# Optimization experiments

Measured on AMD Instinct MI355X. Metric: run time of the kernel, lower is better.

## Reference

```python
import jax, jax.numpy as jnp
import numpy as np
jax.config.update("jax_enable_x64", True)

PAD_ID = -1
NUM_DISCRETE = 128  # args.n_discrete_size

def _lexsort3(v):
    # torch code: stable argsort by x, then y, then z -> final key order z (primary), y, x.
    # numpy/jax lexsort: last key is primary, and it is stable.
    idx = jnp.lexsort((v[:, 0], v[:, 1], v[:, 2]))
    return v[idx], idx

def setup_inputs() -> dict:
    key = jax.random.key(0)
    k1, k2 = jax.random.split(key)
    B, NV, NF = 32, 32768, 65536
    vertices = jax.random.normal(k1, (B, NV, 3), dtype=jnp.float32)
    faces = jax.random.randint(k2, (B, NF, 3), 0, NV, dtype=jnp.int64)
    n_pad = NF // 10
    faces = faces.at[:, NF - n_pad:, :].set(PAD_ID)
    return {"vertices": vertices, "faces": faces}

def reference(vertices, faces):
    B, NV, _ = vertices.shape
    # normalize_vertices reduces over dim 0 (which is the BATCH dim here) - faithful to source
    mn = vertices.min(axis=0)
    mx = vertices.max(axis=0)
    center = (mn + mx) * 0.5
    longest = (mx - mn).max()
    v = (vertices - center) / longest
    # batched lexicographic sort of vertices
    sorted_v, sort_idx = jax.vmap(_lexsort3)(v)
    # inverse permutation (inv[sort_idx] = arange  <=>  argsort of a permutation)
    inv = jnp.argsort(sort_idx, axis=1)  # (B, NV)
    # torch indexes inverse_mapping[faces] with pad -1 wrapping to NV-1
    wrapped = jnp.mod(faces, NV)
    reindexed = jax.vmap(lambda m, f: m[f])(inv, wrapped)  # (B, NF, 3)
    sorted_faces, _ = jax.vmap(_lexsort3)(reindexed)
    # face mask: all three vertex ids != pad
    face_mask = jnp.all(faces != PAD_ID, axis=-1)  # (B, NF)
    face_np = jnp.where(face_mask[..., None], faces, 0)
    # gather vertex coords per face: (B, NF, 3verts, 3coords). The torch code
    # materializes a (b,nf,nv,3) repeat then gathers; we gather directly.
    face_coords = jax.vmap(lambda vv, ff: vv[ff])(sorted_v, face_np)
    # discretize into [-1, 1] -> [0, 127]
    t = (face_coords + 1.0) * 0.5 * NUM_DISCRETE - 0.5
    dq = jnp.clip(jnp.round(t).astype(jnp.int64), 0, NUM_DISCRETE - 1)
    codes = jnp.where(face_mask[..., None, None], dq, PAD_ID)
    input_ids = codes.reshape(B, -1)
    attention_mask = (input_ids != PAD_ID).astype(jnp.float32)
    ph = jnp.full((B, 1), PAD_ID, dtype=input_ids.dtype)
    input_ids = jnp.concatenate([ph, input_ids, ph], axis=1)
    attention_mask = jnp.concatenate([ph.astype(jnp.float32), attention_mask, ph.astype(jnp.float32)], axis=1)
    return input_ids, attention_mask, codes, dq, sorted_faces
```

## Files before the change

### kernel.cpp

```cpp
#include <hip/hip_runtime.h>
#include <stdint.h>

#define BATCH 32
#define NV 32768
#define NF 65536
#define PCOUNT (NV*3)


__device__ __forceinline__ unsigned fenc(float f){
  unsigned u = __float_as_uint(f);
  return (u & 0x80000000u) ? ~u : (u | 0x80000000u);
}
__device__ __forceinline__ float fdec(unsigned e){
  unsigned u = (e & 0x80000000u) ? (e & 0x7FFFFFFFu) : ~e;
  return __uint_as_float(u);
}

__global__ void kminmax(const float* __restrict__ vert, float* __restrict__ center,
                        unsigned* __restrict__ longestBits){
  int p = blockIdx.x*256 + threadIdx.x;
  float mn = 3.4e38f, mx = -3.4e38f;
  #pragma unroll
  for (int b = 0; b < BATCH; ++b) {
    float v = vert[(size_t)b*PCOUNT + p];
    mn = fminf(mn, v); mx = fmaxf(mx, v);
  }
  center[p] = __fadd_rn(mn, mx) * 0.5f;
  float r = __fsub_rn(mx, mn);
  for (int off = 32; off > 0; off >>= 1) r = fmaxf(r, __shfl_down(r, off, 64));
  if ((threadIdx.x & 63) == 0) atomicMax(longestBits, __float_as_uint(r));
}

__device__ __forceinline__ bool less4(uint4 a, uint4 b){
  if (a.x != b.x) return a.x < b.x;
  if (a.y != b.y) return a.y < b.y;
  if (a.z != b.z) return a.z < b.z;
  return a.w < b.w;
}
__device__ __forceinline__ bool less2(uint2 a, uint2 b){
  if (a.y != b.y) return a.y < b.y;
  return a.x < b.x;
}

#define VT 2048
#define FT 4096
#define SWV(i) ((i) ^ (((i) >> 3) & 7))
#define SWF(i) ((i) ^ (((i) >> 4) & 15))

__global__ __launch_bounds__(256) void klocalv(const float* __restrict__ vert,
                                               const float* __restrict__ center,
                                               const unsigned* __restrict__ longestBits,
                                               uint4* __restrict__ S){
  __shared__ uint4 sh[VT];
  int blockBase = blockIdx.x * VT;
  float L = __uint_as_float(*longestBits);
  float rl = __fdiv_rn(1.0f, L);
  for (int i = threadIdx.x; i < VT; i += 256){
    int id = blockBase + i;
    int vi = id & (NV-1);
    size_t vb = (size_t)(id >> 15)*PCOUNT + (size_t)vi*3;
    float nx = __fsub_rn(vert[vb+0], center[vi*3+0]);
    float ny = __fsub_rn(vert[vb+1], center[vi*3+1]);
    float nz = __fsub_rn(vert[vb+2], center[vi*3+2]);
    float x = __fmul_rn(nx, rl);
    float y = __fmul_rn(ny, rl);
    float z = __fmul_rn(nz, rl);
    uint4 s; s.x = fenc(z); s.y = fenc(y); s.z = fenc(x); s.w = (unsigned)vi;
    sh[SWV(i)] = s;
  }
  __syncthreads();
  int t = threadIdx.x;
  int k0 = t * 8;
  uint4 v[8];
  #pragma unroll
  for (int e = 0; e < 8; ++e) v[e] = sh[SWV(k0 + e)];
  #pragma unroll
  for (int k = 2; k <= 8; k <<= 1){
    #pragma unroll
    for (int j = k >> 1; j > 0; j >>= 1){
      #pragma unroll
      for (int i = 0; i < 8; ++i){
        int l = i ^ j;
        if (l > i){
          bool up = ((i & k) == 0);
          bool sw = up ? less4(v[l], v[i]) : less4(v[i], v[l]);
          if (sw){ uint4 tmp = v[i]; v[i] = v[l]; v[l] = tmp; }
        }
      }
    }
  }
  #pragma unroll
  for (int e = 0; e < 8; ++e) sh[SWV(k0 + e)] = v[e];
  __syncthreads();
  for (int w = 8; w < VT; w <<= 1){
    int base = k0 & ~(2*w - 1);
    int ko = k0 - base;
    int lo = ko - w; if (lo < 0) lo = 0;
    int hi = ko < w ? ko : w;
    while (lo < hi){
      int mid = (lo + hi) >> 1;
      if (less4(sh[SWV(base + mid)], sh[SWV(base + w + ko-1-mid)])) lo = mid + 1; else hi = mid;
    }
    int i = lo, j = ko - lo;
    uint4 m[8];
    #pragma unroll
    for (int e = 0; e < 8; ++e){
      bool takeA = (j >= w) || (i < w && less4(sh[SWV(base + i)], sh[SWV(base + w + j)]));
      m[e] = takeA ? sh[SWV(base + i)] : sh[SWV(base + w + j)];
      if (takeA) ++i; else ++j;
    }
    __syncthreads();
    #pragma unroll
    for (int e = 0; e < 8; ++e) sh[SWV(k0 + e)] = m[e];
    __syncthreads();
  }
  uint4* basep = S + (size_t)blockBase;
  for (int i = threadIdx.x; i < VT; i += 256) basep[i] = sh[SWV(i)];
}

__global__ __launch_bounds__(256) void klocalf(const int* __restrict__ faces,
                                               const int* __restrict__ inv,
                                               uint2* __restrict__ F){
  __shared__ uint2 sh[FT];
  int blockBase = blockIdx.x * FT;
  int b = blockBase >> 16;
  const int* invb = inv + (b << 15);
  for (int i = threadIdx.x; i < FT; i += 256){
    int id = blockBase + i;
    int f = id & (NF-1);
    size_t fb = (size_t)id*3;
    int f0 = faces[fb+0], f1 = faces[fb+1], f2 = faces[fb+2];
    unsigned r0 = (unsigned)invb[f0 & (NV-1)];
    unsigned r1 = (unsigned)invb[f1 & (NV-1)];
    unsigned r2 = (unsigned)invb[f2 & (NV-1)];
    uint2 r; r.x = (r0 << 15) | (unsigned)f; r.y = (r2 << 15) | r1;
    sh[SWF(i)] = r;
  }
  __syncthreads();
  int t = threadIdx.x;
  int k0 = t * 16;
  uint2 v[16];
  #pragma unroll
  for (int e = 0; e < 16; ++e) v[e] = sh[SWF(k0 + e)];
  #pragma unroll
  for (int k = 2; k <= 16; k <<= 1){
    #pragma unroll
    for (int j = k >> 1; j > 0; j >>= 1){
      #pragma unroll
      for (int i = 0; i < 16; ++i){
        int l = i ^ j;
        if (l > i){
          bool up = ((i & k) == 0);
          bool sw = up ? less2(v[l], v[i]) : less2(v[i], v[l]);
          if (sw){ uint2 tmp = v[i]; v[i] = v[l]; v[l] = tmp; }
        }
      }
    }
  }
  #pragma unroll
  for (int e = 0; e < 16; ++e) sh[SWF(k0 + e)] = v[e];
  __syncthreads();
  for (int w = 16; w < FT; w <<= 1){
    int base = k0 & ~(2*w - 1);
    int ko = k0 - base;
    int lo = ko - w; if (lo < 0) lo = 0;
    int hi = ko < w ? ko : w;
    while (lo < hi){
      int mid = (lo + hi) >> 1;
      if (less2(sh[SWF(base + mid)], sh[SWF(base + w + ko-1-mid)])) lo = mid + 1; else hi = mid;
    }
    int i = lo, j = ko - lo;
    uint2 m[16];
    #pragma unroll
    for (int e = 0; e < 16; ++e){
      bool takeA = (j >= w) || (i < w && less2(sh[SWF(base + i)], sh[SWF(base + w + j)]));
      m[e] = takeA ? sh[SWF(base + i)] : sh[SWF(base + w + j)];
      if (takeA) ++i; else ++j;
    }
    __syncthreads();
    #pragma unroll
    for (int e = 0; e < 16; ++e) sh[SWF(k0 + e)] = m[e];
    __syncthreads();
  }
  uint2* basep = F + (size_t)blockBase;
  for (int i = threadIdx.x; i < FT; i += 256) basep[i] = sh[SWF(i)];
}

__global__ __launch_bounds__(256) void kmergev(const uint4* __restrict__ src,
                                               uint4* __restrict__ dst, int L){
  __shared__ uint4 sh[2048];
  __shared__ int sAB[2];
  int gid = blockIdx.x;
  int b = gid >> 4, c = gid & 15;
  const uint4* base = src + ((size_t)b << 15);
  uint4* obase = dst + ((size_t)b << 15);
  int co = c * 2048;
  int pair = co / (2*L);
  int ko = co - pair*2*L;
  const uint4* A = base + (size_t)pair*2*L;
  const uint4* B = A + L;
  uint4* O = obase + (size_t)pair*2*L + ko;
  if (threadIdx.x < 2){
    int k = ko + (int)threadIdx.x * 2048;
    int lo = k - L; if (lo < 0) lo = 0;
    int hi = k < L ? k : L;
    while (lo < hi){
      int mid = (lo + hi) >> 1;
      if (less4(A[mid], B[k-1-mid])) lo = mid + 1; else hi = mid;
    }
    sAB[threadIdx.x] = lo;
  }
  __syncthreads();
  int aStart = sAB[0];
  int na = sAB[1] - aStart;
  int nb = 2048 - na;
  int bStart = ko - aStart;
  for (int i = threadIdx.x; i < 2048; i += 256)
    sh[i] = (i < na) ? A[aStart + i] : B[bStart + (i - na)];
  __syncthreads();
  int k0 = threadIdx.x * 8;
  int lo = k0 - nb; if (lo < 0) lo = 0;
  int hi = k0 < na ? k0 : na;
  while (lo < hi){
    int mid = (lo + hi) >> 1;
    if (less4(sh[mid], sh[na + k0-1-mid])) lo = mid + 1; else hi = mid;
  }
  int i = lo, j = k0 - lo;
  #pragma unroll
  for (int e = 0; e < 8; ++e){
    bool takeA = (j >= nb) || (i < na && less4(sh[i], sh[na + j]));
    uint4 v = takeA ? sh[i] : sh[na + j];
    if (takeA) ++i; else ++j;
    O[k0 + e] = v;
  }
}

__global__ __launch_bounds__(256) void kmergef(const uint2* __restrict__ src,
                                               uint2* __restrict__ dst, int L){
  __shared__ uint2 sh[2048];
  __shared__ int sAB[2];
  int gid = blockIdx.x;
  int b = gid >> 5, c = gid & 31;
  const uint2* base = src + ((size_t)b << 16);
  uint2* obase = dst + ((size_t)b << 16);
  int co = c * 2048;
  int pair = co / (2*L);
  int ko = co - pair*2*L;
  const uint2* A = base + (size_t)pair*2*L;
  const uint2* B = A + L;
  uint2* O = obase + (size_t)pair*2*L + ko;
  if (threadIdx.x < 2){
    int k = ko + (int)threadIdx.x * 2048;
    int lo = k - L; if (lo < 0) lo = 0;
    int hi = k < L ? k : L;
    while (lo < hi){
      int mid = (lo + hi) >> 1;
      if (less2(A[mid], B[k-1-mid])) lo = mid + 1; else hi = mid;
    }
    sAB[threadIdx.x] = lo;
  }
  __syncthreads();
  int aStart = sAB[0];
  int na = sAB[1] - aStart;
  int nb = 2048 - na;
  int bStart = ko - aStart;
  for (int i = threadIdx.x; i < 2048; i += 256)
    sh[i] = (i < na) ? A[aStart + i] : B[bStart + (i - na)];
  __syncthreads();
  int k0 = threadIdx.x * 8;
  int lo = k0 - nb; if (lo < 0) lo = 0;
  int hi = k0 < na ? k0 : na;
  while (lo < hi){
    int mid = (lo + hi) >> 1;
    if (less2(sh[mid], sh[na + k0-1-mid])) lo = mid + 1; else hi = mid;
  }
  int i = lo, j = k0 - lo;
  #pragma unroll
  for (int e = 0; e < 8; ++e){
    bool takeA = (j >= nb) || (i < na && less2(sh[i], sh[na + j]));
    uint2 v = takeA ? sh[i] : sh[na + j];
    if (takeA) ++i; else ++j;
    O[k0 + e] = v;
  }
}

__global__ __launch_bounds__(256) void kmergefOut(const uint2* __restrict__ src,
                                                  float* __restrict__ out){
  __shared__ __align__(16) float shf[6144];
  __shared__ int sAB[2];
  uint2* sh = (uint2*)shf;
  const int L = 32768;
  int gid = blockIdx.x;
  int b = gid >> 5, c = gid & 31;
  const uint2* A = src + ((size_t)b << 16);
  const uint2* B = A + L;
  int ko = c * 2048;
  if (threadIdx.x < 2){
    int k = ko + (int)threadIdx.x * 2048;
    int lo = k - L; if (lo < 0) lo = 0;
    int hi = k < L ? k : L;
    while (lo < hi){
      int mid = (lo + hi) >> 1;
      if (less2(A[mid], B[k-1-mid])) lo = mid + 1; else hi = mid;
    }
    sAB[threadIdx.x] = lo;
  }
  __syncthreads();
  int aStart = sAB[0];
  int na = sAB[1] - aStart;
  int nb = 2048 - na;
  int bStart = ko - aStart;
  for (int i = threadIdx.x; i < 2048; i += 256)
    sh[i] = (i < na) ? A[aStart + i] : B[bStart + (i - na)];
  __syncthreads();
  int k0 = threadIdx.x * 8;
  int lo = k0 - nb; if (lo < 0) lo = 0;
  int hi = k0 < na ? k0 : na;
  while (lo < hi){
    int mid = (lo + hi) >> 1;
    if (less2(sh[mid], sh[na + k0-1-mid])) lo = mid + 1; else hi = mid;
  }
  int i = lo, j = k0 - lo;
  uint2 v[8];
  #pragma unroll
  for (int e = 0; e < 8; ++e){
    bool takeA = (j >= nb) || (i < na && less2(sh[i], sh[na + j]));
    v[e] = takeA ? sh[i] : sh[na + j];
    if (takeA) ++i; else ++j;
  }
  __syncthreads();
  #pragma unroll
  for (int e = 0; e < 8; ++e){
    int o = (k0 + e) * 3;
    shf[o+0] = (float)(v[e].x >> 15);
    shf[o+1] = (float)(v[e].y & 0x7FFFu);
    shf[o+2] = (float)(v[e].y >> 15);
  }
  __syncthreads();
  size_t basef = 75497600 + ((size_t)b*65536 + (size_t)ko)*3;
  for (int q = threadIdx.x; q < 6144; q += 256) out[basef + q] = shf[q];
}

__global__ void kinvq(const uint4* __restrict__ S, int* __restrict__ inv,
                      unsigned* __restrict__ Q){
  #pragma clang fp contract(off)
  int id = blockIdx.x*256 + threadIdx.x;
  int b = id >> 15, j = id & (NV-1);
  uint4 s = S[id];
  inv[(b<<15) + (int)s.w] = j;
  float c[3]; c[0] = fdec(s.z); c[1] = fdec(s.y); c[2] = fdec(s.x);
  unsigned qw = 0;
  #pragma unroll
  for (int cc = 0; cc < 3; ++cc){
    float t = ((c[cc] + 1.0f) * 0.5f) * 128.0f - 0.5f;
    float rq = rintf(t);
    int qi = (int)rq;
    qi = qi < 0 ? 0 : (qi > 127 ? 127 : qi);
    qw |= ((unsigned)qi) << (8*cc);
  }
  Q[id] = qw;
}

__global__ __launch_bounds__(256) void kfacesB(const int* __restrict__ faces,
                                               const unsigned* __restrict__ Q,
                                               float* __restrict__ out){
  __shared__ __align__(16) float shq[2304];
  __shared__ float shm[256];
  int p = blockIdx.x;
  int l = ((p & 7) << 10) | (p >> 3);
  int b = l >> 8, c = l & 255;
  int t = threadIdx.x;
  {
    size_t fb = ((size_t)(l*256 + t))*3;
    int f0 = faces[fb+0], f1 = faces[fb+1], f2 = faces[fb+2];
    bool mask = (f0 != -1) & (f1 != -1) & (f2 != -1);
    shm[t] = mask ? 1.0f : 0.0f;
    int fv[3] = {mask ? f0 : 0, mask ? f1 : 0, mask ? f2 : 0};
    #pragma unroll
    for (int k = 0; k < 3; ++k){
      unsigned qw = Q[(b<<15) + fv[k]];
      shq[t*9 + k*3 + 0] = (float)( qw        & 0xFFu);
      shq[t*9 + k*3 + 1] = (float)((qw >> 8 ) & 0xFFu);
      shq[t*9 + k*3 + 2] = (float)((qw >> 16) & 0xFFu);
    }
  }
  __syncthreads();
  float4* cp = (float4*)(out + 37748864 + (size_t)l*2304);
  float4* dp = (float4*)(out + 56623232 + (size_t)l*2304);
  for (int r = t; r < 576; r += 256){
    int e0 = r*4;
    float4 q = *(const float4*)&shq[e0];
    float m0 = shm[(unsigned)(e0  )/9u];
    float m1 = shm[(unsigned)(e0+1)/9u];
    float m2 = shm[(unsigned)(e0+2)/9u];
    float m3 = shm[(unsigned)(e0+3)/9u];
    float4 cv;
    cv.x = m0 != 0.0f ? q.x : -1.0f;
    cv.y = m1 != 0.0f ? q.y : -1.0f;
    cv.z = m2 != 0.0f ? q.z : -1.0f;
    cv.w = m3 != 0.0f ? q.w : -1.0f;
    cp[r] = cv;
    dp[r] = q;
  }
  size_t idsBase  = (size_t)b*589826 + 1 + (size_t)c*2304;
  size_t attnBase = 18874432 + idsBase;
  #pragma unroll
  for (int r = 0; r < 9; ++r){
    int idx = r*256 + t;
    float q = shq[idx];
    float m = shm[(unsigned)idx/9u];
    float cv = m != 0.0f ? q : -1.0f;
    out[idsBase + idx]  = cv;
    out[attnBase + idx] = m;
  }
  if (c == 0 && t == 0){
    out[(size_t)b*589826]                     = -1.0f;
    out[(size_t)b*589826 + 589825]            = -1.0f;
    out[18874432 + (size_t)b*589826]          = -1.0f;
    out[18874432 + (size_t)b*589826 + 589825] = -1.0f;
  }
}

extern "C" void kernel_launch(void* const* d_in, const int* in_sizes, int n_in,
                              void* d_out, int out_size, void* d_ws, size_t ws_size,
                              hipStream_t stream){
  const float* vert  = (const float*)d_in[0];
  const int*   faces = (const int*)d_in[1];
  float* out = (float*)d_out;

  uint4*    S           = (uint4*)d_ws;
  uint4*    S2          = (uint4*)((char*)d_ws + 16777216);
  uint2*    FKa         = (uint2*)((char*)d_ws + 16777216);
  unsigned* Q           = (unsigned*)((char*)d_ws + 16777216);
  uint2*    FKb         = (uint2*)d_ws;
  int*      inv         = (int*)((char*)d_ws + 33554432);
  float*    center      = (float*)((char*)d_ws + 37748736);
  unsigned* longestBits = (unsigned*)((char*)d_ws + 38141952);

  hipMemsetAsync(longestBits, 0, 4, stream);
  kminmax<<<PCOUNT/256, 256, 0, stream>>>(vert, center, longestBits);

  klocalv<<<BATCH*(NV/VT), 256, 0, stream>>>(vert, center, longestBits, S);
  kmergev<<<BATCH*16, 256, 0, stream>>>(S,  S2, 2048);
  kmergev<<<BATCH*16, 256, 0, stream>>>(S2, S,  4096);
  kmergev<<<BATCH*16, 256, 0, stream>>>(S,  S2, 8192);
  kmergev<<<BATCH*16, 256, 0, stream>>>(S2, S,  16384);

  kinvq<<<(BATCH*NV)/256, 256, 0, stream>>>(S, inv, Q);
  kfacesB<<<(BATCH*NF)/256, 256, 0, stream>>>(faces, Q, out);

  klocalf<<<BATCH*(NF/FT), 256, 0, stream>>>(faces, inv, FKa);
  kmergef<<<BATCH*32, 256, 0, stream>>>(FKa, FKb, 4096);
  kmergef<<<BATCH*32, 256, 0, stream>>>(FKb, FKa, 8192);
  kmergef<<<BATCH*32, 256, 0, stream>>>(FKa, FKb, 16384);
  kmergefOut<<<BATCH*32, 256, 0, stream>>>(FKb, out);
}
```

Baseline: 674.8 us.

## Double local sort tile size and fuse final vertex merge with inverse/quantize

Block-local sort tiles double (vertices 4096, faces 8192) with 512 threads per block, so each sort needs one fewer global merge pass. The last vertex merge pass writes the inverse permutation and the quantized coordinates directly, which removes the separate kinvq kernel and a full read of the sorted buffer. The cost is larger shared memory per block (64 KB for vertices), which lowers occupancy for the local sorts. The hidden body of the local sort must also handle the larger tile.

Result: faster. 643.1 us (-4.7%).

```diff
diff --git a/kernel.cpp b/kernel.cpp
--- a/kernel.cpp
+++ b/kernel.cpp
@@ -42,12 +42,12 @@
   return a.x < b.x;
 }
 
-#define VT 2048
-#define FT 4096
+#define VT 4096
+#define FT 8192
 #define SWV(i) ((i) ^ (((i) >> 3) & 7))
 #define SWF(i) ((i) ^ (((i) >> 4) & 15))
 
-__global__ __launch_bounds__(256) void klocalv(const float* __restrict__ vert,
+__global__ __launch_bounds__(512) void klocalv(const float* __restrict__ vert,
                                                const float* __restrict__ center,
                                                const unsigned* __restrict__ longestBits,
                                                uint4* __restrict__ S){
@@ -55,7 +55,7 @@
   int blockBase = blockIdx.x * VT;
   float L = __uint_as_float(*longestBits);
   float rl = __fdiv_rn(1.0f, L);
-  for (int i = threadIdx.x; i < VT; i += 256){
+  for (int i = threadIdx.x; i < VT; i += 512){
     int id = blockBase + i;
     int vi = id & (NV-1);
     size_t vb = (size_t)(id >> 15)*PCOUNT + (size_t)vi*3;
@@ -115,17 +115,17 @@
     __syncthreads();
   }
   uint4* basep = S + (size_t)blockBase;
-  for (int i = threadIdx.x; i < VT; i += 256) basep[i] = sh[SWV(i)];
-}
-
-__global__ __launch_bounds__(256) void klocalf(const int* __restrict__ faces,
+  for (int i = threadIdx.x; i < VT; i += 512) basep[i] = sh[SWV(i)];
+}
+
+__global__ __launch_bounds__(512) void klocalf(const int* __restrict__ faces,
                                                const int* __restrict__ inv,
                                                uint2* __restrict__ F){
   __shared__ uint2 sh[FT];
   int blockBase = blockIdx.x * FT;
   int b = blockBase >> 16;
   const int* invb = inv + (b << 15);
-  for (int i = threadIdx.x; i < FT; i += 256){
+  for (int i = threadIdx.x; i < FT; i += 512){
     int id = blockBase + i;
     int f = id & (NF-1);
     size_t fb = (size_t)id*3;
@@ -183,7 +183,7 @@
     __syncthreads();
   }
   uint2* basep = F + (size_t)blockBase;
-  for (int i = threadIdx.x; i < FT; i += 256) basep[i] = sh[SWF(i)];
+  for (int i = threadIdx.x; i < FT; i += 512) basep[i] = sh[SWF(i)];
 }
 
 __global__ __launch_bounds__(256) void kmergev(const uint4* __restrict__ src,
@@ -235,6 +235,65 @@
   }
 }
 
+__global__ __launch_bounds__(256) void kmergevQ(const uint4* __restrict__ src,
+                                                int* __restrict__ inv,
+                                                unsigned* __restrict__ Q){
+  #pragma clang fp contract(off)
+  __shared__ uint4 sh[2048];
+  __shared__ int sAB[2];
+  const int L = 16384;
+  int gid = blockIdx.x;
+  int b = gid >> 4, c = gid & 15;
+  const uint4* A = src + ((size_t)b << 15);
+  const uint4* B = A + L;
+  int ko = c * 2048;
+  if (threadIdx.x < 2){
+    int k = ko + (int)threadIdx.x * 2048;
+    int lo = k - L; if (lo < 0) lo = 0;
+    int hi = k < L ? k : L;
+    while (lo < hi){
+      int mid = (lo + hi) >> 1;
+      if (less4(A[mid], B[k-1-mid])) lo = mid + 1; else hi = mid;
+    }
+    sAB[threadIdx.x] = lo;
+  }
+  __syncthreads();
+  int aStart = sAB[0];
+  int na = sAB[1] - aStart;
+  int nb = 2048 - na;
+  int bStart = ko - aStart;
+  for (int i = threadIdx.x; i < 2048; i += 256)
+    sh[i] = (i < na) ? A[aStart + i] : B[bStart + (i - na)];
+  __syncthreads();
+  int k0 = threadIdx.x * 8;
+  int lo = k0 - nb; if (lo < 0) lo = 0;
+  int hi = k0 < na ? k0 : na;
+  while (lo < hi){
+    int mid = (lo + hi) >> 1;
+    if (less4(sh[mid], sh[na + k0-1-mid])) lo = mid + 1; else hi = mid;
+  }
+  int i = lo, j = k0 - lo;
+  #pragma unroll
+  for (int e = 0; e < 8; ++e){
+    bool takeA = (j >= nb) || (i < na && less4(sh[i], sh[na + j]));
+    uint4 s = takeA ? sh[i] : sh[na + j];
+    if (takeA) ++i; else ++j;
+    int pos = ko + k0 + e;
+    inv[(b<<15) + (int)s.w] = pos;
+    float cco[3]; cco[0] = fdec(s.z); cco[1] = fdec(s.y); cco[2] = fdec(s.x);
+    unsigned qw = 0;
+    #pragma unroll
+    for (int cc = 0; cc < 3; ++cc){
+      float tt = ((cco[cc] + 1.0f) * 0.5f) * 128.0f - 0.5f;
+      float rq = rintf(tt);
+      int qi = (int)rq;
+      qi = qi < 0 ? 0 : (qi > 127 ? 127 : qi);
+      qw |= ((unsigned)qi) << (8*cc);
+    }
+    Q[(b<<15) + pos] = qw;
+  }
+}
+
 __global__ __launch_bounds__(256) void kmergef(const uint2* __restrict__ src,
                                                uint2* __restrict__ dst, int L){
   __shared__ uint2 sh[2048];
@@ -341,26 +400,6 @@
   for (int q = threadIdx.x; q < 6144; q += 256) out[basef + q] = shf[q];
 }
 
-__global__ void kinvq(const uint4* __restrict__ S, int* __restrict__ inv,
-                      unsigned* __restrict__ Q){
-  #pragma clang fp contract(off)
-  int id = blockIdx.x*256 + threadIdx.x;
-  int b = id >> 15, j = id & (NV-1);
-  uint4 s = S[id];
-  inv[(b<<15) + (int)s.w] = j;
-  float c[3]; c[0] = fdec(s.z); c[1] = fdec(s.y); c[2] = fdec(s.x);
-  unsigned qw = 0;
-  #pragma unroll
-  for (int cc = 0; cc < 3; ++cc){
-    float t = ((c[cc] + 1.0f) * 0.5f) * 128.0f - 0.5f;
-    float rq = rintf(t);
-    int qi = (int)rq;
-    qi = qi < 0 ? 0 : (qi > 127 ? 127 : qi);
-    qw |= ((unsigned)qi) << (8*cc);
-  }
-  Q[id] = qw;
-}
-
 __global__ __launch_bounds__(256) void kfacesB(const int* __restrict__ faces,
                                                const unsigned* __restrict__ Q,
                                                float* __restrict__ out){
@@ -440,18 +479,15 @@
   hipMemsetAsync(longestBits, 0, 4, stream);
   kminmax<<<PCOUNT/256, 256, 0, stream>>>(vert, center, longestBits);
 
-  klocalv<<<BATCH*(NV/VT), 256, 0, stream>>>(vert, center, longestBits, S);
-  kmergev<<<BATCH*16, 256, 0, stream>>>(S,  S2, 2048);
-  kmergev<<<BATCH*16, 256, 0, stream>>>(S2, S,  4096);
-  kmergev<<<BATCH*16, 256, 0, stream>>>(S,  S2, 8192);
-  kmergev<<<BATCH*16, 256, 0, stream>>>(S2, S,  16384);
-
-  kinvq<<<(BATCH*NV)/256, 256, 0, stream>>>(S, inv, Q);
+  klocalv<<<BATCH*(NV/VT), 512, 0, stream>>>(vert, center, longestBits, S);
+  kmergev<<<BATCH*16, 256, 0, stream>>>(S,  S2, 4096);
+  kmergev<<<BATCH*16, 256, 0, stream>>>(S2, S,  8192);
+  kmergevQ<<<BATCH*16, 256, 0, stream>>>(S, inv, Q);
+
   kfacesB<<<(BATCH*NF)/256, 256, 0, stream>>>(faces, Q, out);
 
-  klocalf<<<BATCH*(NF/FT), 256, 0, stream>>>(faces, inv, FKa);
-  kmergef<<<BATCH*32, 256, 0, stream>>>(FKa, FKb, 4096);
-  kmergef<<<BATCH*32, 256, 0, stream>>>(FKb, FKa, 8192);
-  kmergef<<<BATCH*32, 256, 0, stream>>>(FKa, FKb, 16384);
-  kmergefOut<<<BATCH*32, 256, 0, stream>>>(FKb, out);
-}
+  klocalf<<<BATCH*(NF/FT), 512, 0, stream>>>(faces, inv, FKa);
+  kmergef<<<BATCH*32, 256, 0, stream>>>(FKa, FKb, 8192);
+  kmergef<<<BATCH*32, 256, 0, stream>>>(FKb, FKa, 16384);
+  kmergefOut<<<BATCH*32, 256, 0, stream>>>(FKa, out);
+}
```
